# Performance work log

Measured on AMD Instinct MI355X. Metric: run time of the kernel, lower is better.

## Reference

```python
import jax, jax.numpy as jnp
import numpy as np

B, LT, LS, D, H, F = 4, 1024, 1024, 1024, 16, 4096
HD = D // H
EPS = 1e-6


def rms_norm(x, g):
    return x / jnp.sqrt(jnp.mean(x * x, axis=-1, keepdims=True) + EPS) * g


def mha(q_in, kv_in, wq, wk, wv, wo, bias):
    # q_in: [B,Lq,D], kv_in: [B,Lk,D], bias broadcastable to [B,H,Lq,Lk]
    b, lq, _ = q_in.shape
    lk = kv_in.shape[1]
    q = (q_in @ wq).reshape(b, lq, H, HD).transpose(0, 2, 1, 3)
    k = (kv_in @ wk).reshape(b, lk, H, HD).transpose(0, 2, 1, 3)
    v = (kv_in @ wv).reshape(b, lk, H, HD).transpose(0, 2, 1, 3)
    s = jnp.einsum('bhqd,bhkd->bhqk', q, k) / np.sqrt(HD).astype(np.float32) + bias
    o = jnp.einsum('bhqk,bhkd->bhqd', jax.nn.softmax(s, axis=-1), v)
    o = o.transpose(0, 2, 1, 3).reshape(b, lq, D) @ wo
    return o, k, v


def setup_inputs() -> dict:
    key = jax.random.key(0)
    ks = jax.random.split(key, 16)
    f = lambda k, sh, s: jax.random.normal(k, sh, jnp.float32) * s
    wscale = 1.0 / float(np.sqrt(D))
    causal = jnp.where(jnp.triu(jnp.ones((LT, LT), bool), 1), jnp.float32(-1e9), jnp.float32(0.0))
    return {
        'x': f(ks[0], (B, LT, D), 1.0),
        'memory': f(ks[1], (B, LS, D), 1.0),
        'position_embedding': f(ks[2], (1, H, LT, LS), 0.02),
        'causal_mask': causal,
        'gamma_sa': jnp.ones((D,), jnp.float32),
        'wq_s': f(ks[3], (D, D), wscale), 'wk_s': f(ks[4], (D, D), wscale),
        'wv_s': f(ks[5], (D, D), wscale), 'wo_s': f(ks[6], (D, D), wscale),
        'gamma_ca': jnp.ones((D,), jnp.float32),
        'wq_c': f(ks[7], (D, D), wscale), 'wk_c': f(ks[8], (D, D), wscale),
        'wv_c': f(ks[9], (D, D), wscale), 'wo_c': f(ks[10], (D, D), wscale),
        'gamma_m': jnp.ones((D,), jnp.float32),
        'w1': f(ks[11], (D, F), wscale), 'w2': f(ks[12], (F, D), 1.0 / float(np.sqrt(F))),
    }


def reference(x, memory, position_embedding, causal_mask,
              gamma_sa, wq_s, wk_s, wv_s, wo_s,
              gamma_ca, wq_c, wk_c, wv_c, wo_c,
              gamma_m, w1, w2):
    # self-attention block (pre-RMSNorm, causal mask, residual)
    h = rms_norm(x, gamma_sa)
    a, k_s, v_s = mha(h, h, wq_s, wk_s, wv_s, wo_s, causal_mask[None, None, :, :])
    attn_x = a + x
    # cross-attention block (position-embedding bias on scores, residual)
    h2 = rms_norm(attn_x, gamma_ca)
    c, k_c, v_c = mha(h2, memory, wq_c, wk_c, wv_c, wo_c, position_embedding)
    cross_x = c + attn_x
    # FFN block
    h3 = rms_norm(cross_x, gamma_m)
    mlp_x = jax.nn.relu(h3 @ w1) @ w2 + cross_x
    return mlp_x, (k_s, v_s), (k_c, v_c)
```

## Files before the change

### kernel.cpp

```cpp
#include <hip/hip_runtime.h>
#include <stdint.h>
#include <stddef.h>

typedef __bf16 bf16_t;
typedef __attribute__((ext_vector_type(8))) __bf16 bf16x8;
typedef __attribute__((ext_vector_type(4))) float f32x4;

#define LT 1024
#define LS 1024
#define DM 1024
#define NH 16
#define HD 64
#define FF 4096
#define BB 4

__device__ __forceinline__ void gld_lds16(const bf16_t* g, bf16_t* l) {
    __builtin_amdgcn_global_load_lds(
        (const __attribute__((address_space(1))) void*)g,
        (__attribute__((address_space(3))) void*)l, 16, 0, 0);
}

__global__ __launch_bounds__(256) void transpose_f2bf(
    const float* __restrict__ in, bf16_t* __restrict__ out, int R, int C)
{
    __shared__ float tile[32][33];
    int bx = blockIdx.x * 32;
    int by = blockIdx.y * 32;
    int tx = threadIdx.x, ty = threadIdx.y;
#pragma unroll
    for (int j = 0; j < 4; j++)
        tile[ty + j * 8][tx] = in[(size_t)(by + ty + j * 8) * C + bx + tx];
    __syncthreads();
#pragma unroll
    for (int j = 0; j < 4; j++)
        out[(size_t)(bx + ty + j * 8) * R + by + tx] = (bf16_t)tile[tx][ty + j * 8];
}

__global__ __launch_bounds__(256) void f2bf_kernel(
    const float* __restrict__ in, bf16_t* __restrict__ out, size_t n)
{
    size_t i = ((size_t)blockIdx.x * 256 + threadIdx.x) * 4;
    if (i + 3 < n) {
        float4 v = *(const float4*)&in[i];
        out[i + 0] = (bf16_t)v.x;
        out[i + 1] = (bf16_t)v.y;
        out[i + 2] = (bf16_t)v.z;
        out[i + 3] = (bf16_t)v.w;
    }
}

__global__ __launch_bounds__(256) void rmsnorm_kernel(
    const float* __restrict__ x, const float* __restrict__ g,
    bf16_t* __restrict__ out)
{
    __shared__ float red[4];
    int row = blockIdx.x;
    int t = threadIdx.x;
    int lane = t & 63, w = t >> 6;
    const float* xr = x + (size_t)row * DM;
    float4 v = *(const float4*)&xr[t * 4];
    float ss = v.x * v.x + v.y * v.y + v.z * v.z + v.w * v.w;
#pragma unroll
    for (int off = 32; off > 0; off >>= 1) ss += __shfl_down(ss, off, 64);
    if (lane == 0) red[w] = ss;
    __syncthreads();
    float tot = red[0] + red[1] + red[2] + red[3];
    float inv = rsqrtf(tot * (1.0f / DM) + 1e-6f);
    float4 gv = *(const float4*)&g[t * 4];
    bf16_t* o = out + (size_t)row * DM + t * 4;
    o[0] = (bf16_t)(v.x * inv * gv.x);
    o[1] = (bf16_t)(v.y * inv * gv.y);
    o[2] = (bf16_t)(v.z * inv * gv.z);
    o[3] = (bf16_t)(v.w * inv * gv.w);
}

#define EP_QKV 0
#define EP_RES 1
#define EP_RELU 2

template <int EP, int KSPLIT>
__global__ __launch_bounds__(256) void gemm_bt(
    const bf16_t* __restrict__ A, const bf16_t* __restrict__ Bt,
    int N, int K, int sec_base,
    float* __restrict__ outF, bf16_t* __restrict__ outB,
    bf16_t* __restrict__ qb,
    float* __restrict__ kF, bf16_t* __restrict__ kB,
    float* __restrict__ vF, bf16_t* __restrict__ vB)
{
    __shared__ bf16_t lA[128 * 64];
    __shared__ bf16_t lB[128 * 64];
    const int t = threadIdx.x;
    const int lane = t & 63, w = t >> 6;
    const int quad = lane >> 4, l15 = lane & 15;
    const int m0 = blockIdx.x * 128, n0 = blockIdx.y * 128;
    const int wr = w >> 1, wc = w & 1;
    const int Kc = K / KSPLIT;
    const int kBeg = blockIdx.z * Kc, kEnd = kBeg + Kc;

    f32x4 acc[4][4] = {};

    for (int k0 = kBeg; k0 < kEnd; k0 += 64) {
        __syncthreads();
#pragma unroll
        for (int i = 0; i < 4; i++) {
            int p = i * 256 + t;
            int row = p >> 3;
            int g = (p & 7) ^ (row & 7);
            gld_lds16(&A[(size_t)(m0 + row) * K + k0 + g * 8], &lA[p * 8]);
            gld_lds16(&Bt[(size_t)(n0 + row) * K + k0 + g * 8], &lB[p * 8]);
        }
        __syncthreads();
#pragma unroll
        for (int s = 0; s < 2; s++) {
            bf16x8 af[4], bfr[4];
#pragma unroll
            for (int mt = 0; mt < 4; mt++) {
                int r = wr * 64 + mt * 16 + l15;
                af[mt] = *(const bf16x8*)&lA[((r << 3) + ((s * 4 + quad) ^ (r & 7))) << 3];
            }
#pragma unroll
            for (int nt = 0; nt < 4; nt++) {
                int r = wc * 64 + nt * 16 + l15;
                bfr[nt] = *(const bf16x8*)&lB[((r << 3) + ((s * 4 + quad) ^ (r & 7))) << 3];
            }
#pragma unroll
            for (int mt = 0; mt < 4; mt++)
#pragma unroll
                for (int nt = 0; nt < 4; nt++)
                    acc[mt][nt] = __builtin_amdgcn_mfma_f32_16x16x32_bf16(
                        af[mt], bfr[nt], acc[mt][nt], 0, 0, 0);
        }
    }

#pragma unroll
    for (int mt = 0; mt < 4; mt++) {
#pragma unroll
        for (int nt = 0; nt < 4; nt++) {
#pragma unroll
            for (int r = 0; r < 4; r++) {
                int row = m0 + wr * 64 + mt * 16 + quad * 4 + r;
                int col = n0 + wc * 64 + nt * 16 + l15;
                float v = acc[mt][nt][r];
                if constexpr (EP == EP_RES) {
                    atomicAdd(&outF[(size_t)row * N + col], v);
                } else if constexpr (EP == EP_RELU) {
                    outB[(size_t)row * N + col] = (bf16_t)fmaxf(v, 0.0f);
                } else {
                    int b = row >> 10, tp = row & 1023;
                    int c10 = col & 1023;
                    int sec = (col >> 10) + sec_base;
                    int h = c10 >> 6, d = c10 & 63;
                    size_t hb = ((size_t)(b * NH + h)) << 16;
                    if (sec == 0) {
                        qb[hb + (size_t)tp * HD + d] = (bf16_t)v;
                    } else if (sec == 1) {
                        kF[hb + (size_t)tp * HD + d] = v;
                        kB[hb + (size_t)tp * HD + d] = (bf16_t)v;
                    } else {
                        vF[hb + (size_t)tp * HD + d] = v;
                        vB[hb + (size_t)d * LT + tp] = (bf16_t)v;
                    }
                }
            }
        }
    }
}

template <bool CAUSAL>
__global__ __launch_bounds__(256) void flash_attn(
    const bf16_t* __restrict__ Q, const bf16_t* __restrict__ Kb,
    const bf16_t* __restrict__ Vt, const float* __restrict__ bias,
    bf16_t* __restrict__ O)
{
    __shared__ bf16_t lK[64 * 64];
    __shared__ bf16_t lV[64 * 64];
    __shared__ bf16_t lP[4][16 * 64];
    const int t = threadIdx.x;
    const int lane = t & 63, w = t >> 6;
    const int quad = lane >> 4, l15 = lane & 15;
    const int qt = blockIdx.x;
    const int bh = blockIdx.y;
    const int b = bh >> 4, h = bh & 15;
    const int q0 = qt * 64;

    const bf16_t* qbase = Q + (size_t)bh * LT * HD;
    const bf16_t* kbase = Kb + (size_t)bh * LS * HD;
    const bf16_t* vbase = Vt + (size_t)bh * HD * LS;

    bf16x8 qf[2];
    int qrow = q0 + w * 16 + l15;
#pragma unroll
    for (int s = 0; s < 2; s++)
        qf[s] = *(const bf16x8*)&qbase[(size_t)qrow * HD + s * 32 + quad * 8];

    f32x4 acc_o[4] = {};
    float m_i[4], l_i[4];
#pragma unroll
    for (int r = 0; r < 4; r++) { m_i[r] = -3.0e38f; l_i[r] = 0.0f; }

    const int nkt = CAUSAL ? (qt + 1) : (LS / 64);
    for (int kt = 0; kt < nkt; kt++) {
        const int kb = kt * 64;
        __syncthreads();
#pragma unroll
        for (int i = 0; i < 2; i++) {
            int p = i * 256 + t;
            int row = p >> 3;
            int g = (p & 7) ^ (row & 7);
            gld_lds16(&kbase[(size_t)(kb + row) * HD + g * 8], &lK[p * 8]);
            gld_lds16(&vbase[(size_t)row * LS + kb + g * 8], &lV[p * 8]);
        }
        __syncthreads();

        f32x4 sacc[4];
#pragma unroll
        for (int nt = 0; nt < 4; nt++) {
            f32x4 sa = {};
#pragma unroll
            for (int s = 0; s < 2; s++) {
                int r = nt * 16 + l15;
                bf16x8 kf = *(const bf16x8*)&lK[((r << 3) + ((s * 4 + quad) ^ (r & 7))) << 3];
                sa = __builtin_amdgcn_mfma_f32_16x16x32_bf16(qf[s], kf, sa, 0, 0, 0);
            }
            sacc[nt] = sa;
        }

        float sval[4][4];
        float tmax[4];
#pragma unroll
        for (int r = 0; r < 4; r++) tmax[r] = -3.0e38f;
#pragma unroll
        for (int nt = 0; nt < 4; nt++) {
            int col = kb + nt * 16 + l15;
#pragma unroll
            for (int r = 0; r < 4; r++) {
                int row = q0 + w * 16 + quad * 4 + r;
                float v = sacc[nt][r] * 0.125f;
                if constexpr (CAUSAL) {
                    if (col > row) v = -1e9f;
                } else {
                    v += bias[((size_t)(h * LT + row)) * LS + col];
                }
                sval[nt][r] = v;
                tmax[r] = fmaxf(tmax[r], v);
            }
        }
#pragma unroll
        for (int r = 0; r < 4; r++) {
            float v = tmax[r];
            v = fmaxf(v, __shfl_xor(v, 1, 64));
            v = fmaxf(v, __shfl_xor(v, 2, 64));
            v = fmaxf(v, __shfl_xor(v, 4, 64));
            v = fmaxf(v, __shfl_xor(v, 8, 64));
            tmax[r] = v;
        }
        float alpha[4], rsum[4];
#pragma unroll
        for (int r = 0; r < 4; r++) {
            float mn = fmaxf(m_i[r], tmax[r]);
            alpha[r] = __expf(m_i[r] - mn);
            m_i[r] = mn;
            rsum[r] = 0.0f;
        }
#pragma unroll
        for (int nt = 0; nt < 4; nt++) {
#pragma unroll
            for (int r = 0; r < 4; r++) {
                float p = __expf(sval[nt][r] - m_i[r]);
                rsum[r] += p;
                int pr = quad * 4 + r;
                int gcol = nt * 2 + (l15 >> 3);
                lP[w][((pr << 3) + (gcol ^ (pr & 7))) * 8 + (l15 & 7)] = (bf16_t)p;
            }
        }
#pragma unroll
        for (int r = 0; r < 4; r++) {
            float v = rsum[r];
            v += __shfl_xor(v, 1, 64);
            v += __shfl_xor(v, 2, 64);
            v += __shfl_xor(v, 4, 64);
            v += __shfl_xor(v, 8, 64);
            l_i[r] = l_i[r] * alpha[r] + v;
        }
#pragma unroll
        for (int dt = 0; dt < 4; dt++)
#pragma unroll
            for (int r = 0; r < 4; r++)
                acc_o[dt][r] *= alpha[r];

#pragma unroll
        for (int s = 0; s < 2; s++) {
            bf16x8 pf = *(const bf16x8*)&lP[w][((l15 << 3) + ((s * 4 + quad) ^ (l15 & 7))) << 3];
#pragma unroll
            for (int dt = 0; dt < 4; dt++) {
                int r = dt * 16 + l15;
                bf16x8 vf = *(const bf16x8*)&lV[((r << 3) + ((s * 4 + quad) ^ (r & 7))) << 3];
                acc_o[dt] = __builtin_amdgcn_mfma_f32_16x16x32_bf16(pf, vf, acc_o[dt], 0, 0, 0);
            }
        }
    }

#pragma unroll
    for (int dt = 0; dt < 4; dt++) {
#pragma unroll
        for (int r = 0; r < 4; r++) {
            int row = q0 + w * 16 + quad * 4 + r;
            int col = h * HD + dt * 16 + l15;
            float v = acc_o[dt][r] / l_i[r];
            O[((size_t)(b * LT + row)) * DM + col] = (bf16_t)v;
        }
    }
}

extern "C" void kernel_launch(void* const* d_in, const int* in_sizes, int n_in,
                              void* d_out, int out_size, void* d_ws, size_t ws_size,
                              hipStream_t stream)
{
    (void)in_sizes; (void)n_in; (void)out_size; (void)ws_size;
    const float* x    = (const float*)d_in[0];
    const float* mem  = (const float*)d_in[1];
    const float* pemb = (const float*)d_in[2];
    const float* g_sa = (const float*)d_in[4];
    const float* wq_s = (const float*)d_in[5];
    const float* wk_s = (const float*)d_in[6];
    const float* wv_s = (const float*)d_in[7];
    const float* wo_s = (const float*)d_in[8];
    const float* g_ca = (const float*)d_in[9];
    const float* wq_c = (const float*)d_in[10];
    const float* wk_c = (const float*)d_in[11];
    const float* wv_c = (const float*)d_in[12];
    const float* wo_c = (const float*)d_in[13];
    const float* g_m  = (const float*)d_in[14];
    const float* w1   = (const float*)d_in[15];
    const float* w2   = (const float*)d_in[16];
    float* out = (float*)d_out;

    const size_t OFF_KS = 4u * 1024 * 1024;
    const size_t OFF_VS = 8u * 1024 * 1024;
    const size_t OFF_KC = 12u * 1024 * 1024;
    const size_t OFF_VC = 16u * 1024 * 1024;

    char* ws = (char*)d_ws;
    const size_t MB = 1024 * 1024;
    bf16_t* wqkvTs = (bf16_t*)(ws + 0 * MB);
    bf16_t* woTs   = (bf16_t*)(ws + 6 * MB);
    bf16_t* wqTc   = (bf16_t*)(ws + 8 * MB);
    bf16_t* wkvTc  = (bf16_t*)(ws + 10 * MB);
    bf16_t* woTc   = (bf16_t*)(ws + 14 * MB);
    bf16_t* w1T    = (bf16_t*)(ws + 16 * MB);
    bf16_t* w2T    = (bf16_t*)(ws + 24 * MB);
    bf16_t* membf  = (bf16_t*)(ws + 32 * MB);
    bf16_t* hbuf   = (bf16_t*)(ws + 40 * MB);
    bf16_t* qbuf   = (bf16_t*)(ws + 48 * MB);
    bf16_t* kbuf   = (bf16_t*)(ws + 56 * MB);
    bf16_t* vTbuf  = (bf16_t*)(ws + 64 * MB);
    bf16_t* Obuf   = (bf16_t*)(ws + 72 * MB);
    float*  attn_x  = (float*)(ws + 80 * MB);
    float*  cross_x = (float*)(ws + 96 * MB);
    bf16_t* ffnmid  = (bf16_t*)(ws + 112 * MB);

    dim3 tb(32, 8);
    transpose_f2bf<<<dim3(32, 32), tb, 0, stream>>>(wq_s, wqkvTs, DM, DM);
    transpose_f2bf<<<dim3(32, 32), tb, 0, stream>>>(wk_s, wqkvTs + 1024 * 1024, DM, DM);
    transpose_f2bf<<<dim3(32, 32), tb, 0, stream>>>(wv_s, wqkvTs + 2 * 1024 * 1024, DM, DM);
    transpose_f2bf<<<dim3(32, 32), tb, 0, stream>>>(wo_s, woTs, DM, DM);
    transpose_f2bf<<<dim3(32, 32), tb, 0, stream>>>(wq_c, wqTc, DM, DM);
    transpose_f2bf<<<dim3(32, 32), tb, 0, stream>>>(wk_c, wkvTc, DM, DM);
    transpose_f2bf<<<dim3(32, 32), tb, 0, stream>>>(wv_c, wkvTc + 1024 * 1024, DM, DM);
    transpose_f2bf<<<dim3(32, 32), tb, 0, stream>>>(wo_c, woTc, DM, DM);
    transpose_f2bf<<<dim3(128, 32), tb, 0, stream>>>(w1, w1T, DM, FF);
    transpose_f2bf<<<dim3(32, 128), tb, 0, stream>>>(w2, w2T, FF, DM);

    f2bf_kernel<<<4096, 256, 0, stream>>>(mem, membf, (size_t)BB * LS * DM);

    const size_t ROWB = (size_t)BB * LT * DM * sizeof(float);

    rmsnorm_kernel<<<BB * LT, 256, 0, stream>>>(x, g_sa, hbuf);
    gemm_bt<EP_QKV, 1><<<dim3(32, 24), 256, 0, stream>>>(
        hbuf, wqkvTs, 3072, 1024, 0, nullptr, nullptr,
        qbuf, out + OFF_KS, kbuf, out + OFF_VS, vTbuf);
    flash_attn<true><<<dim3(16, 64), 256, 0, stream>>>(qbuf, kbuf, vTbuf, nullptr, Obuf);
    hipMemcpyAsync(attn_x, x, ROWB, hipMemcpyDeviceToDevice, stream);
    gemm_bt<EP_RES, 1><<<dim3(32, 8), 256, 0, stream>>>(
        Obuf, woTs, 1024, 1024, 0, attn_x, nullptr,
        nullptr, nullptr, nullptr, nullptr, nullptr);

    rmsnorm_kernel<<<BB * LT, 256, 0, stream>>>(attn_x, g_ca, hbuf);
    gemm_bt<EP_QKV, 1><<<dim3(32, 8), 256, 0, stream>>>(
        hbuf, wqTc, 1024, 1024, 0, nullptr, nullptr,
        qbuf, nullptr, nullptr, nullptr, nullptr);
    gemm_bt<EP_QKV, 1><<<dim3(32, 16), 256, 0, stream>>>(
        membf, wkvTc, 2048, 1024, 1, nullptr, nullptr,
        nullptr, out + OFF_KC, kbuf, out + OFF_VC, vTbuf);
    flash_attn<false><<<dim3(16, 64), 256, 0, stream>>>(qbuf, kbuf, vTbuf, pemb, Obuf);
    hipMemcpyAsync(cross_x, attn_x, ROWB, hipMemcpyDeviceToDevice, stream);
    gemm_bt<EP_RES, 1><<<dim3(32, 8), 256, 0, stream>>>(
        Obuf, woTc, 1024, 1024, 0, cross_x, nullptr,
        nullptr, nullptr, nullptr, nullptr, nullptr);

    rmsnorm_kernel<<<BB * LT, 256, 0, stream>>>(cross_x, g_m, hbuf);
    gemm_bt<EP_RELU, 1><<<dim3(32, 32), 256, 0, stream>>>(
        hbuf, w1T, 4096, 1024, 0, nullptr, ffnmid,
        nullptr, nullptr, nullptr, nullptr, nullptr);
    hipMemcpyAsync(out, cross_x, ROWB, hipMemcpyDeviceToDevice, stream);
    gemm_bt<EP_RES, 4><<<dim3(32, 8, 4), 256, 0, stream>>>(
        ffnmid, w2T, 1024, 4096, 0, out, nullptr,
        nullptr, nullptr, nullptr, nullptr, nullptr);
}
```

Measured before the change: 722.6 us.

## Replace atomic residual adds and memcpys with fused residual epilogues and split-K partials

The output-projection GEMMs now add the residual in the epilogue and write plain stores, which removes the device-to-device memcpys and the fp32 atomicAdd traffic. The FFN down-projection moves from 4-way split-K with atomics to 2-way split-K writing partial buffers, followed by a separate reduce kernel that also adds the residual. The cross-attention Q and KV projections are merged into one launch. The strided V-transpose scatter in the QKV epilogue is replaced by coalesced stores plus a separate tiled transpose kernel. The cost is extra kernels and extra buffer traffic, and workspace buffers are now reused with overlapping regions.

```diff
diff --git a/kernel.cpp b/kernel.cpp
--- a/kernel.cpp
+++ b/kernel.cpp
@@ -36,6 +36,25 @@
         out[(size_t)(bx + ty + j * 8) * R + by + tx] = (bf16_t)tile[tx][ty + j * 8];
 }
 
+__global__ __launch_bounds__(256) void transpose_bf(
+    const bf16_t* __restrict__ in, bf16_t* __restrict__ out)
+{
+    __shared__ bf16_t tile[32][33];
+    int bh = blockIdx.z;
+    int r0 = blockIdx.x * 32;
+    int c0 = blockIdx.y * 32;
+    const bf16_t* ib = in + (size_t)bh * LT * HD;
+    bf16_t* ob = out + (size_t)bh * HD * LT;
+    int tx = threadIdx.x, ty = threadIdx.y;
+#pragma unroll
+    for (int j = 0; j < 4; j++)
+        tile[ty + j * 8][tx] = ib[(size_t)(r0 + ty + j * 8) * HD + c0 + tx];
+    __syncthreads();
+#pragma unroll
+    for (int j = 0; j < 4; j++)
+        ob[(size_t)(c0 + ty + j * 8) * LT + r0 + tx] = tile[tx][ty + j * 8];
+}
+
 __global__ __launch_bounds__(256) void f2bf_kernel(
     const float* __restrict__ in, bf16_t* __restrict__ out, size_t n)
 {
@@ -47,6 +66,21 @@
         out[i + 2] = (bf16_t)v.z;
         out[i + 3] = (bf16_t)v.w;
     }
+}
+
+__global__ __launch_bounds__(256) void reduce2_res(
+    const float* __restrict__ p, const float* __restrict__ res,
+    float* __restrict__ out)
+{
+    const size_t MN = (size_t)BB * LT * DM;
+    size_t i = ((size_t)blockIdx.x * 256 + threadIdx.x) * 4;
+    float4 a = *(const float4*)&p[i];
+    float4 b = *(const float4*)&p[i + MN];
+    float4 r = *(const float4*)&res[i];
+    float4 o;
+    o.x = a.x + b.x + r.x; o.y = a.y + b.y + r.y;
+    o.z = a.z + b.z + r.z; o.w = a.w + b.w + r.w;
+    *(float4*)&out[i] = o;
 }
 
 __global__ __launch_bounds__(256) void rmsnorm_kernel(
@@ -74,18 +108,102 @@
     o[3] = (bf16_t)(v.w * inv * gv.w);
 }
 
-#define EP_QKV 0
-#define EP_RES 1
-#define EP_RELU 2
+#define GEMM_BODY(Aptr, Btptr, Kstride, kBeg, kEnd)                              \
+    for (int k0 = (kBeg); k0 < (kEnd); k0 += 64) {                               \
+        __syncthreads();                                                         \
+        _Pragma("unroll")                                                        \
+        for (int i = 0; i < 4; i++) {                                            \
+            int p = i * 256 + t;                                                 \
+            int row = p >> 3;                                                    \
+            int g = (p & 7) ^ (row & 7);                                         \
+            gld_lds16(&(Aptr)[(size_t)(m0 + row) * (Kstride) + k0 + g * 8],      \
+                      &lA[p * 8]);                                               \
+            gld_lds16(&(Btptr)[(size_t)(n0 + row) * (Kstride) + k0 + g * 8],     \
+                      &lB[p * 8]);                                               \
+        }                                                                        \
+        __syncthreads();                                                         \
+        _Pragma("unroll")                                                        \
+        for (int s = 0; s < 2; s++) {                                            \
+            bf16x8 af[4], bfr[4];                                                \
+            _Pragma("unroll")                                                    \
+            for (int mt = 0; mt < 4; mt++) {                                     \
+                int r = wr * 64 + mt * 16 + l15;                                 \
+                af[mt] = *(const bf16x8*)&lA[((r << 3) + ((s * 4 + quad) ^ (r & 7))) << 3]; \
+            }                                                                    \
+            _Pragma("unroll")                                                    \
+            for (int nt = 0; nt < 4; nt++) {                                     \
+                int r = wc * 64 + nt * 16 + l15;                                 \
+                bfr[nt] = *(const bf16x8*)&lB[((r << 3) + ((s * 4 + quad) ^ (r & 7))) << 3]; \
+            }                                                                    \
+            _Pragma("unroll")                                                    \
+            for (int mt = 0; mt < 4; mt++)                                       \
+                _Pragma("unroll")                                                \
+                for (int nt = 0; nt < 4; nt++)                                   \
+                    acc[mt][nt] = __builtin_amdgcn_mfma_f32_16x16x32_bf16(       \
+                        af[mt], bfr[nt], acc[mt][nt], 0, 0, 0);                  \
+        }                                                                        \
+    }
+
+__global__ __launch_bounds__(256) void gemm_qkv(
+    const bf16_t* __restrict__ A1, const bf16_t* __restrict__ B1, int nb1,
+    const bf16_t* __restrict__ A2, const bf16_t* __restrict__ B2, int secbase2,
+    bf16_t* __restrict__ qb,
+    float* __restrict__ kF, bf16_t* __restrict__ kB,
+    float* __restrict__ vF, bf16_t* __restrict__ vB)
+{
+    __shared__ bf16_t lA[128 * 64];
+    __shared__ bf16_t lB[128 * 64];
+    const int t = threadIdx.x;
+    const int lane = t & 63, w = t >> 6;
+    const int quad = lane >> 4, l15 = lane & 15;
+    const int m0 = blockIdx.x * 128;
+    const int wr = w >> 1, wc = w & 1;
+
+    const bf16_t* A; const bf16_t* Bt; int n0, sec0;
+    if ((int)blockIdx.y < nb1) { A = A1; Bt = B1; n0 = blockIdx.y * 128; sec0 = 0; }
+    else { A = A2; Bt = B2; n0 = (blockIdx.y - nb1) * 128; sec0 = secbase2; }
+
+    f32x4 acc[4][4] = {};
+    GEMM_BODY(A, Bt, 1024, 0, 1024)
+
+#pragma unroll
+    for (int mt = 0; mt < 4; mt++) {
+#pragma unroll
+        for (int nt = 0; nt < 4; nt++) {
+#pragma unroll
+            for (int r = 0; r < 4; r++) {
+                int row = m0 + wr * 64 + mt * 16 + quad * 4 + r;
+                int col = n0 + wc * 64 + nt * 16 + l15;
+                float v = acc[mt][nt][r];
+                int b = row >> 10, tp = row & 1023;
+                int sec = sec0 + (col >> 10);
+                int c10 = col & 1023;
+                int h = c10 >> 6, d = c10 & 63;
+                size_t idx = (((size_t)(b * NH + h)) << 16) + (size_t)tp * HD + d;
+                if (sec == 0) {
+                    qb[idx] = (bf16_t)v;
+                } else if (sec == 1) {
+                    kF[idx] = v;
+                    kB[idx] = (bf16_t)v;
+                } else {
+                    vF[idx] = v;
+                    vB[idx] = (bf16_t)v;
+                }
+            }
+        }
+    }
+}
+
+#define EP_RES 0
+#define EP_RELU 1
+#define EP_PART 2
 
 template <int EP, int KSPLIT>
 __global__ __launch_bounds__(256) void gemm_bt(
     const bf16_t* __restrict__ A, const bf16_t* __restrict__ Bt,
-    int N, int K, int sec_base,
-    float* __restrict__ outF, bf16_t* __restrict__ outB,
-    bf16_t* __restrict__ qb,
-    float* __restrict__ kF, bf16_t* __restrict__ kB,
-    float* __restrict__ vF, bf16_t* __restrict__ vB)
+    int N, int K,
+    float* __restrict__ outF, const float* __restrict__ res,
+    bf16_t* __restrict__ outB)
 {
     __shared__ bf16_t lA[128 * 64];
     __shared__ bf16_t lB[128 * 64];
@@ -95,42 +213,14 @@
     const int m0 = blockIdx.x * 128, n0 = blockIdx.y * 128;
     const int wr = w >> 1, wc = w & 1;
     const int Kc = K / KSPLIT;
-    const int kBeg = blockIdx.z * Kc, kEnd = kBeg + Kc;
+    const int kBeg = blockIdx.z * Kc;
 
     f32x4 acc[4][4] = {};
-
-    for (int k0 = kBeg; k0 < kEnd; k0 += 64) {
-        __syncthreads();
-#pragma unroll
-        for (int i = 0; i < 4; i++) {
-            int p = i * 256 + t;
-            int row = p >> 3;
-            int g = (p & 7) ^ (row & 7);
-            gld_lds16(&A[(size_t)(m0 + row) * K + k0 + g * 8], &lA[p * 8]);
-            gld_lds16(&Bt[(size_t)(n0 + row) * K + k0 + g * 8], &lB[p * 8]);
-        }
-        __syncthreads();
-#pragma unroll
-        for (int s = 0; s < 2; s++) {
-            bf16x8 af[4], bfr[4];
-#pragma unroll
-            for (int mt = 0; mt < 4; mt++) {
-                int r = wr * 64 + mt * 16 + l15;
-                af[mt] = *(const bf16x8*)&lA[((r << 3) + ((s * 4 + quad) ^ (r & 7))) << 3];
-            }
-#pragma unroll
-            for (int nt = 0; nt < 4; nt++) {
-                int r = wc * 64 + nt * 16 + l15;
-                bfr[nt] = *(const bf16x8*)&lB[((r << 3) + ((s * 4 + quad) ^ (r & 7))) << 3];
-            }
-#pragma unroll
-            for (int mt = 0; mt < 4; mt++)
-#pragma unroll
-                for (int nt = 0; nt < 4; nt++)
-                    acc[mt][nt] = __builtin_amdgcn_mfma_f32_16x16x32_bf16(
-                        af[mt], bfr[nt], acc[mt][nt], 0, 0, 0);
-        }
-    }
+    GEMM_BODY(A, Bt, K, kBeg, kBeg + Kc)
+
+    float* dst = outF;
+    if constexpr (EP == EP_PART)
+        dst = outF + (size_t)blockIdx.z * (size_t)gridDim.x * 128 * N;
 
 #pragma unroll
     for (int mt = 0; mt < 4; mt++) {
@@ -142,24 +232,11 @@
                 int col = n0 + wc * 64 + nt * 16 + l15;
                 float v = acc[mt][nt][r];
                 if constexpr (EP == EP_RES) {
-                    atomicAdd(&outF[(size_t)row * N + col], v);
+                    dst[(size_t)row * N + col] = v + res[(size_t)row * N + col];
                 } else if constexpr (EP == EP_RELU) {
                     outB[(size_t)row * N + col] = (bf16_t)fmaxf(v, 0.0f);
                 } else {
-                    int b = row >> 10, tp = row & 1023;
-                    int c10 = col & 1023;
-                    int sec = (col >> 10) + sec_base;
-                    int h = c10 >> 6, d = c10 & 63;
-                    size_t hb = ((size_t)(b * NH + h)) << 16;
-                    if (sec == 0) {
-                        qb[hb + (size_t)tp * HD + d] = (bf16_t)v;
-                    } else if (sec == 1) {
-                        kF[hb + (size_t)tp * HD + d] = v;
-                        kB[hb + (size_t)tp * HD + d] = (bf16_t)v;
-                    } else {
-                        vF[hb + (size_t)tp * HD + d] = v;
-                        vB[hb + (size_t)d * LT + tp] = (bf16_t)v;
-                    }
+                    dst[(size_t)row * N + col] = v;
                 }
             }
         }
@@ -353,11 +430,13 @@
     bf16_t* hbuf   = (bf16_t*)(ws + 40 * MB);
     bf16_t* qbuf   = (bf16_t*)(ws + 48 * MB);
     bf16_t* kbuf   = (bf16_t*)(ws + 56 * MB);
-    bf16_t* vTbuf  = (bf16_t*)(ws + 64 * MB);
-    bf16_t* Obuf   = (bf16_t*)(ws + 72 * MB);
-    float*  attn_x  = (float*)(ws + 80 * MB);
-    float*  cross_x = (float*)(ws + 96 * MB);
-    bf16_t* ffnmid  = (bf16_t*)(ws + 112 * MB);
+    bf16_t* vbuf   = (bf16_t*)(ws + 64 * MB);
+    bf16_t* vTbuf  = (bf16_t*)(ws + 72 * MB);
+    bf16_t* Obuf   = (bf16_t*)(ws + 80 * MB);
+    float*  attn_x  = (float*)(ws + 88 * MB);
+    float*  cross_x = (float*)(ws + 112 * MB);
+    bf16_t* ffnmid  = (bf16_t*)(ws + 48 * MB);
+    float*  part    = (float*)(ws + 80 * MB);
 
     dim3 tb(32, 8);
     transpose_f2bf<<<dim3(32, 32), tb, 0, stream>>>(wq_s, wqkvTs, DM, DM);
@@ -373,37 +452,28 @@
 
     f2bf_kernel<<<4096, 256, 0, stream>>>(mem, membf, (size_t)BB * LS * DM);
 
-    const size_t ROWB = (size_t)BB * LT * DM * sizeof(float);
-
     rmsnorm_kernel<<<BB * LT, 256, 0, stream>>>(x, g_sa, hbuf);
-    gemm_bt<EP_QKV, 1><<<dim3(32, 24), 256, 0, stream>>>(
-        hbuf, wqkvTs, 3072, 1024, 0, nullptr, nullptr,
-        qbuf, out + OFF_KS, kbuf, out + OFF_VS, vTbuf);
+    gemm_qkv<<<dim3(32, 24), 256, 0, stream>>>(
+        hbuf, wqkvTs, 24, hbuf, wqkvTs, 0,
+        qbuf, out + OFF_KS, kbuf, out + OFF_VS, vbuf);
+    transpose_bf<<<dim3(32, 2, 64), tb, 0, stream>>>(vbuf, vTbuf);
     flash_attn<true><<<dim3(16, 64), 256, 0, stream>>>(qbuf, kbuf, vTbuf, nullptr, Obuf);
-    hipMemcpyAsync(attn_x, x, ROWB, hipMemcpyDeviceToDevice, stream);
     gemm_bt<EP_RES, 1><<<dim3(32, 8), 256, 0, stream>>>(
-        Obuf, woTs, 1024, 1024, 0, attn_x, nullptr,
-        nullptr, nullptr, nullptr, nullptr, nullptr);
+        Obuf, woTs, 1024, 1024, attn_x, x, nullptr);
 
     rmsnorm_kernel<<<BB * LT, 256, 0, stream>>>(attn_x, g_ca, hbuf);
-    gemm_bt<EP_QKV, 1><<<dim3(32, 8), 256, 0, stream>>>(
-        hbuf, wqTc, 1024, 1024, 0, nullptr, nullptr,
-        qbuf, nullptr, nullptr, nullptr, nullptr);
-    gemm_bt<EP_QKV, 1><<<dim3(32, 16), 256, 0, stream>>>(
-        membf, wkvTc, 2048, 1024, 1, nullptr, nullptr,
-        nullptr, out + OFF_KC, kbuf, out + OFF_VC, vTbuf);
+    gemm_qkv<<<dim3(32, 24), 256, 0, stream>>>(
+        hbuf, wqTc, 8, membf, wkvTc, 1,
+        qbuf, out + OFF_KC, kbuf, out + OFF_VC, vbuf);
+    transpose_bf<<<dim3(32, 2, 64), tb, 0, stream>>>(vbuf, vTbuf);
     flash_attn<false><<<dim3(16, 64), 256, 0, stream>>>(qbuf, kbuf, vTbuf, pemb, Obuf);
-    hipMemcpyAsync(cross_x, attn_x, ROWB, hipMemcpyDeviceToDevice, stream);
     gemm_bt<EP_RES, 1><<<dim3(32, 8), 256, 0, stream>>>(
-        Obuf, woTc, 1024, 1024, 0, cross_x, nullptr,
-        nullptr, nullptr, nullptr, nullptr, nullptr);
+        Obuf, woTc, 1024, 1024, cross_x, attn_x, nullptr);
 
     rmsnorm_kernel<<<BB * LT, 256, 0, stream>>>(cross_x, g_m, hbuf);
     gemm_bt<EP_RELU, 1><<<dim3(32, 32), 256, 0, stream>>>(
-        hbuf, w1T, 4096, 1024, 0, nullptr, ffnmid,
-        nullptr, nullptr, nullptr, nullptr, nullptr);
-    hipMemcpyAsync(out, cross_x, ROWB, hipMemcpyDeviceToDevice, stream);
-    gemm_bt<EP_RES, 4><<<dim3(32, 8, 4), 256, 0, stream>>>(
-        ffnmid, w2T, 1024, 4096, 0, out, nullptr,
-        nullptr, nullptr, nullptr, nullptr, nullptr);
-}
+        hbuf, w1T, 4096, 1024, nullptr, nullptr, ffnmid);
+    gemm_bt<EP_PART, 2><<<dim3(32, 8, 2), 256, 0, stream>>>(
+        ffnmid, w2T, 1024, 4096, part, nullptr, nullptr);
+    reduce2_res<<<4096, 256, 0, stream>>>(part, cross_x, out);
+}
```

Measured after the change: 654.9 us. -9.4%, faster.
